# Optimization experiments

Measured on AMD Instinct MI355X. Metric: run time of the kernel, lower is better.

Reference implementation:

```python
import jax, jax.numpy as jnp
import numpy as np
import math

NH, DH, BS, LOCAL, RAND, NCLS = 12, 64, 49, 3, 3, 1
WINDOW = (8, 14, 14)
NKV = LOCAL + RAND


def make_rel_pos_index():
    ws = WINDOW
    rel_size = [2 * w - 1 for w in ws]
    coords = np.stack(np.meshgrid(*[np.arange(w) for w in ws], indexing='ij')).reshape(len(ws), -1)
    rel = (coords[:, :, None] - coords[:, None, :]).transpose(1, 2, 0).astype(np.int64)
    for i, w in enumerate(ws):
        rel[:, :, i] += w - 1
    for i, r in enumerate(rel_size[1:]):
        rel[:, :, :i + 1] *= r
    n = coords.shape[1]
    S = n + NCLS
    idx = np.zeros((S, S), dtype=np.int64)
    idx[NCLS:, NCLS:] = rel.sum(-1)
    start = int(np.prod(rel_size))
    idx[:NCLS, NCLS:] = np.arange(NCLS)[:, None] + start
    start += NCLS
    idx[NCLS:, :NCLS] = np.arange(NCLS)[None, :] + start
    start += NCLS
    idx[:NCLS, :NCLS] = np.arange(NCLS ** 2).reshape(NCLS, NCLS) + start
    return idx.astype(np.int32)


def setup_inputs() -> dict:
    key = jax.random.key(0)
    ks = jax.random.split(key, 8)
    B, S, D = 8, 1569, 768
    M = (S - NCLS) // BS  # 32 blocks
    hidden_states = jax.random.normal(ks[0], (B, S, D), dtype=jnp.float32)
    Wq = jax.random.normal(ks[1], (D, D), dtype=jnp.float32) * 0.02
    bq = jax.random.normal(ks[2], (D,), dtype=jnp.float32) * 0.02
    Wk = jax.random.normal(ks[3], (D, D), dtype=jnp.float32) * 0.02
    Wv = jax.random.normal(ks[4], (D, D), dtype=jnp.float32) * 0.02
    bv = jax.random.normal(ks[5], (D,), dtype=jnp.float32) * 0.02
    rel_table = jax.random.normal(ks[6], (10938, NH), dtype=jnp.float32) * 0.02
    rel_pos_index = jnp.asarray(make_rel_pos_index())
    rand_idx = jnp.sort(jax.random.randint(ks[7], (M, RAND), 0, M), axis=1).astype(jnp.int32)
    return {"hidden_states": hidden_states, "Wq": Wq, "bq": bq, "Wk": Wk, "Wv": Wv,
            "bv": bv, "rel_table": rel_table, "rel_pos_index": rel_pos_index, "rand_idx": rand_idx}


def reference(hidden_states, Wq, bq, Wk, Wv, bv, rel_table, rel_pos_index, rand_idx):
    B, S, D = hidden_states.shape
    scale = 1.0 / math.sqrt(DH)
    q = hidden_states @ Wq + bq
    k = hidden_states @ Wk          # key has no bias in BeitSelfAttention
    v = hidden_states @ Wv + bv
    split = lambda x: x.reshape(B, S, NH, DH).transpose(0, 2, 1, 3)  # b h s d
    q, k, v = split(q), split(k), split(v)

    # --- dense attention for cls queries over all keys ---
    cls_q = q[:, :, :NCLS]
    sim_cls = jnp.einsum('bhid,bhjd->bhij', cls_q, k) * scale
    bias_cls = rel_table[rel_pos_index[:NCLS, :]]           # [ncls, S, H]
    sim_cls = sim_cls + bias_cls.transpose(2, 0, 1)[None]
    attn_cls = jax.nn.softmax(sim_cls, axis=-1)
    out_cls = jnp.einsum('bhij,bhjd->bhid', attn_cls, v)    # [B,H,ncls,DH]

    # --- block-sparse attention for local queries ---
    loc_q = q[:, :, NCLS:]
    cls_k, loc_k = k[:, :, :NCLS], k[:, :, NCLS:]
    cls_v, loc_v = v[:, :, :NCLS], v[:, :, NCLS:]
    N = S - NCLS
    M = N // BS  # evenly divisible -> pad_q = 0
    qb = loc_q.reshape(B, NH, M, BS, DH)
    kb = loc_k.reshape(B, NH, M, BS, DH)
    vb = loc_v.reshape(B, NH, M, BS, DH)

    # local + random key-block indices per query block: [M, NKV]
    offs = jnp.arange(-(LOCAL // 2), LOCAL // 2 + 1)
    local_idx = (jnp.arange(M)[:, None] + offs[None, :]) % M
    attn_idx = jnp.concatenate([local_idx.astype(jnp.int32), rand_idx], axis=1)

    kg = kb[:, :, attn_idx]   # [B,H,M,NKV,BS,DH]
    vg = vb[:, :, attn_idx]

    sim_loc = jnp.einsum('bhmid,bhmnjd->bhminj', qb, kg).reshape(B, NH, M, BS, NKV * BS)
    sim_c = jnp.einsum('bhmid,bhjd->bhmij', qb, cls_k)       # [B,H,M,BS,ncls]
    sim = jnp.concatenate([sim_c, sim_loc], axis=-1) * scale

    # gathered relative-position bias: query tokens are ncls..S-1 in order
    key_tok = (NCLS + attn_idx[:, :, None] * BS + jnp.arange(BS)[None, None, :]).reshape(M, NKV * BS)
    to_idx = jnp.concatenate([jnp.broadcast_to(jnp.arange(NCLS)[None], (M, NCLS)), key_tok], axis=1)
    q_rows = rel_pos_index[NCLS:].reshape(M, BS, S)
    bias_idx = jnp.take_along_axis(q_rows, jnp.broadcast_to(to_idx[:, None, :], (M, BS, to_idx.shape[1])), axis=-1)
    bias = rel_table[bias_idx]                                # [M,BS,ncls+NKV*BS,H]
    sim = sim + bias.transpose(3, 0, 1, 2)[None]

    attn = jax.nn.softmax(sim, axis=-1)
    a_cls = attn[..., :NCLS]
    a_loc = attn[..., NCLS:].reshape(B, NH, M, BS, NKV, BS)
    out_loc = jnp.einsum('bhminj,bhmnjd->bhmid', a_loc, vg) \
            + jnp.einsum('bhmic,bhcd->bhmid', a_cls, cls_v)
    out_loc = out_loc.reshape(B, NH, N, DH)

    out = jnp.concatenate([out_cls, out_loc], axis=2)         # [B,H,S,DH]
    return out.transpose(0, 2, 1, 3).reshape(B, S, D)
```

## Files before the change

### kernel.cpp

```cpp
#include <hip/hip_runtime.h>


#define S_TOT   1569
#define NBATCH  8

__global__ __launch_bounds__(256) void gemm_f32(const float* __restrict__ hs,
                                                const float* __restrict__ Wq,
                                                const float* __restrict__ Wk,
                                                const float* __restrict__ Wv,
                                                const float* __restrict__ bq,
                                                const float* __restrict__ bv,
                                                float* __restrict__ Q,
                                                float* __restrict__ K,
                                                float* __restrict__ V,
                                                int b0, int nTok) {
    __shared__ float As[128][20];
    __shared__ float Bs[16][136];
    int tid = threadIdx.x;
    int t0 = blockIdx.x * 128;
    int n0 = blockIdx.y * 128;
    int which = n0 / 768;
    int ng0 = n0 - which * 768;
    const float* W = (which == 0) ? Wq : (which == 1 ? Wk : Wv);
    const float* Xb = hs + (size_t)b0 * S_TOT * 768;

    int tr = tid >> 4;
    int tc = tid & 15;

    int sat = tid >> 2;
    int sac4 = (tid & 3) * 4;
    int sbk = tid >> 4;
    int sbn = (tid & 15) * 4;

    int scg = ((tid & 3) ^ ((sat >> 3) & 3)) * 4;
    int rswz = (tr & 3);

    int ta0 = t0 + sat;       if (ta0 >= nTok) ta0 = nTok - 1;
    int ta1 = t0 + sat + 64;  if (ta1 >= nTok) ta1 = nTok - 1;

    float acc[8][8];
#pragma unroll
    for (int i = 0; i < 8; i++)
#pragma unroll
        for (int j = 0; j < 8; j++) acc[i][j] = 0.f;

    float4 pa0, pa1, pb0, pb1;
    {
        pa0 = *(const float4*)(Xb + (size_t)ta0 * 768 + 0 + sac4);
        pa1 = *(const float4*)(Xb + (size_t)ta1 * 768 + 0 + sac4);
        const float* wr_ = W + (size_t)(0 + sbk) * 768 + ng0;
        pb0 = *(const float4*)(wr_ + sbn);
        pb1 = *(const float4*)(wr_ + 64 + sbn);
    }

    for (int k0 = 0; k0 < 768; k0 += 16) {
        *(float4*)&As[sat][scg]      = pa0;
        *(float4*)&As[sat + 64][scg] = pa1;
        *(float4*)&Bs[sbk][sbn]      = pb0;
        *(float4*)&Bs[sbk][64 + sbn] = pb1;
        __syncthreads();

        if (k0 + 16 < 768) {
            int kn = k0 + 16;
            pa0 = *(const float4*)(Xb + (size_t)ta0 * 768 + kn + sac4);
            pa1 = *(const float4*)(Xb + (size_t)ta1 * 768 + kn + sac4);
            const float* wr_ = W + (size_t)(kn + sbk) * 768 + ng0;
            pb0 = *(const float4*)(wr_ + sbn);
            pb1 = *(const float4*)(wr_ + 64 + sbn);
        }

#pragma unroll
        for (int kq = 0; kq < 4; kq++) {
            float4 xa[8];
            int rc = (kq ^ rswz) * 4;
#pragma unroll
            for (int i = 0; i < 8; i++)
                xa[i] = *(const float4*)&As[tr * 8 + i][rc];
#pragma unroll
            for (int kk = 0; kk < 4; kk++) {
                int k = kq * 4 + kk;
                float4 w0 = *(const float4*)&Bs[k][tc * 4];
                float4 w1 = *(const float4*)&Bs[k][64 + tc * 4];
#pragma unroll
                for (int i = 0; i < 8; i++) {
                    float a = (kk == 0) ? xa[i].x : (kk == 1) ? xa[i].y
                            : (kk == 2) ? xa[i].z : xa[i].w;
                    acc[i][0] = fmaf(a, w0.x, acc[i][0]);
                    acc[i][1] = fmaf(a, w0.y, acc[i][1]);
                    acc[i][2] = fmaf(a, w0.z, acc[i][2]);
                    acc[i][3] = fmaf(a, w0.w, acc[i][3]);
                    acc[i][4] = fmaf(a, w1.x, acc[i][4]);
                    acc[i][5] = fmaf(a, w1.y, acc[i][5]);
                    acc[i][6] = fmaf(a, w1.z, acc[i][6]);
                    acc[i][7] = fmaf(a, w1.w, acc[i][7]);
                }
            }
        }
        __syncthreads();
    }

    float* dst = (which == 0) ? Q : (which == 1 ? K : V);
    const float* bias = (which == 0) ? bq : (which == 2 ? bv : nullptr);
#pragma unroll
    for (int hh = 0; hh < 2; hh++) {
        int nn = ng0 + hh * 64 + tc * 4;
        int h = nn >> 6, d = nn & 63;
        float4 bv4 = make_float4(0.f, 0.f, 0.f, 0.f);
        if (bias) bv4 = *(const float4*)(bias + nn);
#pragma unroll
        for (int i = 0; i < 8; i++) {
            int t = t0 + tr * 8 + i;
            if (t >= nTok) continue;
            int bl = t / S_TOT;
            int s = t - bl * S_TOT;
            float4 o;
            o.x = acc[i][hh * 4 + 0] + bv4.x;
            o.y = acc[i][hh * 4 + 1] + bv4.y;
            o.z = acc[i][hh * 4 + 2] + bv4.z;
            o.w = acc[i][hh * 4 + 3] + bv4.w;
            *(float4*)(dst + ((size_t)(bl * 12 + h) * S_TOT + s) * 64 + d) = o;
        }
    }
}

__global__ __launch_bounds__(256) void cls_attn(const float* __restrict__ Q,
                                                const float* __restrict__ K,
                                                const float* __restrict__ V,
                                                const float* __restrict__ rel,
                                                const int* __restrict__ rpi,
                                                float* __restrict__ out, int b0) {
    int bh = blockIdx.x;
    int bl = bh / 12, h = bh - bl * 12;
    __shared__ float p[S_TOT];
    __shared__ float4 qs4[16];
    __shared__ float red[256];
    __shared__ float wred[8];
    int tid = threadIdx.x, lane = tid & 63, w = tid >> 6;
    size_t base = (size_t)bh * S_TOT * 64;
    const float* Qb = Q + base;
    const float* Kb = K + base;
    const float* Vb = V + base;
    if (tid < 64) ((float*)qs4)[tid] = Qb[tid];
    __syncthreads();

    float lmx = -1e30f;
    for (int j = tid; j < S_TOT; j += 256) {
        const float4* kr = (const float4*)(Kb + j * 64);
        float a = 0.f;
#pragma unroll
        for (int d4 = 0; d4 < 16; d4++) {
            float4 kv = kr[d4];
            float4 qv = qs4[d4];
            a = fmaf(qv.x, kv.x, a); a = fmaf(qv.y, kv.y, a);
            a = fmaf(qv.z, kv.z, a); a = fmaf(qv.w, kv.w, a);
        }
        a = a * 0.125f + rel[rpi[j] * 12 + h];
        p[j] = a;
        lmx = fmaxf(lmx, a);
    }
#pragma unroll
    for (int off = 32; off > 0; off >>= 1) lmx = fmaxf(lmx, __shfl_xor(lmx, off));
    if (lane == 0) wred[w] = lmx;
    __syncthreads();
    float mx = fmaxf(fmaxf(wred[0], wred[1]), fmaxf(wred[2], wred[3]));
    float lsum = 0.f;
    for (int j = tid; j < S_TOT; j += 256) {
        float e = __expf(p[j] - mx);
        p[j] = e;
        lsum += e;
    }
#pragma unroll
    for (int off = 32; off > 0; off >>= 1) lsum += __shfl_xor(lsum, off);
    if (lane == 0) wred[4 + w] = lsum;
    __syncthreads();
    float inv = 1.0f / (wred[4] + wred[5] + wred[6] + wred[7]);
    float acc = 0.f;
    for (int j = w; j < S_TOT; j += 4) acc = fmaf(p[j], Vb[j * 64 + lane], acc);
    red[w * 64 + lane] = acc;
    __syncthreads();
    if (w == 0) {
        float o = (red[lane] + red[64 + lane] + red[128 + lane] + red[192 + lane]) * inv;
        out[(size_t)(b0 + bl) * S_TOT * 768 + h * 64 + lane] = o;
    }
}

__global__ __launch_bounds__(256, 4) void loc_attn(const float* __restrict__ Q,
                                                   const float* __restrict__ K,
                                                   const float* __restrict__ V,
                                                   const float* __restrict__ rel,
                                                   const int* __restrict__ rand_idx,
                                                   float* __restrict__ out,
                                                   int b0, int ng) {
    int d = blockIdx.x;
    int xcd = d & 7, kk_ = d >> 3;
    int slot = xcd * (ng << 2) + kk_;
    int g = slot >> 5;
    int m = slot & 31;
    int h = g % 12;
    int bl = g / 12;

    __shared__ float Qlds[49][64];
    __shared__ float Plds[4][13][64];
    __shared__ float flds[4][13][5];
    __shared__ int   cqlds[52];
    __shared__ unsigned short tok[320];
    int tid = threadIdx.x, lane = tid & 63, w = tid >> 6;

    size_t base = (size_t)((bl * 12 + h) * S_TOT) * 64;
    const float* Qb = Q + base;
    const float* Kb = K + base;
    const float* Vb = V + base;

    for (int jj = tid; jj < 320; jj += 256) {
        int t = 0;
        if (jj >= 1 && jj < 295) {
            int j1 = jj - 1;
            int n = j1 / 49;
            int q = j1 - n * 49;
            int a;
            if (n == 0)      a = (m + 31) & 31;
            else if (n == 1) a = m;
            else if (n == 2) a = (m + 1) & 31;
            else             a = rand_idx[m * 3 + (n - 3)];
            t = 1 + a * 49 + q;
        }
        tok[jj] = (unsigned short)t;
    }
    if (tid < 52) {
        int qr = 1 + m * 49 + tid;
        if (qr > S_TOT - 1) qr = S_TOT - 1;
        int pq = qr - 1;
        int zq = pq / 196;
        int rem = pq - zq * 196;
        int yq = rem / 14;
        int xq = rem - yq * 14;
        cqlds[tid] = zq * 729 + yq * 27 + xq;
    }
    for (int idx = tid; idx < 49 * 64; idx += 256) {
        int r = idx >> 6, c = idx & 63;
        ((float*)Qlds)[idx] = Qb[(size_t)(1 + m * 49 + r) * 64 + c];
    }
    __syncthreads();

    float facc[13];
#pragma unroll
    for (int r = 0; r < 13; r++) facc[r] = 0.f;

    for (int jc = 0; jc < 5; jc++) {
        int j = jc * 64 + lane;
        int tj = tok[j];
        const float* kp = Kb + (size_t)tj * 64;

        int pj = tj - 1;
        int zj = pj / 196;
        int remj = pj - zj * 196;
        int yj = remj / 14;
        int xj = remj - yj * 14;
        int cjb = 5467 - (zj * 729 + yj * 27 + xj);
        bool iscls = (tj == 0);
        bool jv = j < 295;

#pragma unroll
        for (int half = 0; half < 2; half++) {
            const int r0 = half * 7;
            const int RN = half ? 6 : 7;
            float s[7];
#pragma unroll
            for (int rr = 0; rr < 7; rr++) s[rr] = 0.f;
#pragma unroll 4
            for (int d4 = 0; d4 < 16; d4++) {
                float4 kv = *(const float4*)(kp + d4 * 4);
#pragma unroll
                for (int rr = 0; rr < RN; rr++) {
                    int qrow = w + 4 * (r0 + rr);
                    if (qrow > 48) qrow = 48;
                    float4 qv = *(const float4*)&Qlds[qrow][d4 * 4];
                    s[rr] = fmaf(qv.x, kv.x, s[rr]);
                    s[rr] = fmaf(qv.y, kv.y, s[rr]);
                    s[rr] = fmaf(qv.z, kv.z, s[rr]);
                    s[rr] = fmaf(qv.w, kv.w, s[rr]);
                }
            }
#pragma unroll
            for (int rr = 0; rr < RN; rr++) {
                int r = r0 + rr;
                int i = w + 4 * r;
                int ii = (i > 48) ? 48 : i;
                int bidx = iscls ? 10936 : (cqlds[ii] + cjb);
                float e = jv ? __expf(fmaf(s[rr], 0.125f, rel[bidx * 12 + h])) : 0.f;
                float ps = e;
#pragma unroll
                for (int off = 32; off > 0; off >>= 1) ps += __shfl_xor(ps, off);
                if (lane == 0) flds[w][r][jc] = ps;
                Plds[w][r][lane] = e;
            }
        }

#pragma unroll 4
        for (int jg = 0; jg < 16; jg++) {
            int jb = jc * 64 + jg * 4;
            int t0 = tok[jb + 0], t1 = tok[jb + 1], t2 = tok[jb + 2], t3 = tok[jb + 3];
            float v0 = Vb[(size_t)t0 * 64 + lane];
            float v1 = Vb[(size_t)t1 * 64 + lane];
            float v2 = Vb[(size_t)t2 * 64 + lane];
            float v3 = Vb[(size_t)t3 * 64 + lane];
#pragma unroll
            for (int r = 0; r < 13; r++) {
                float4 p4 = *(const float4*)&Plds[w][r][jg * 4];
                facc[r] = fmaf(p4.x, v0, facc[r]);
                facc[r] = fmaf(p4.y, v1, facc[r]);
                facc[r] = fmaf(p4.z, v2, facc[r]);
                facc[r] = fmaf(p4.w, v3, facc[r]);
            }
        }
    }

    int nrows = (w == 0) ? 13 : 12;
    for (int r = 0; r < nrows; r++) {
        float fl = ((flds[w][r][0] + flds[w][r][1]) + (flds[w][r][2] + flds[w][r][3]))
                 + flds[w][r][4];
        int i = w + 4 * r;
        int st = 1 + m * 49 + i;
        out[((size_t)(b0 + bl) * S_TOT + st) * 768 + h * 64 + lane] = facc[r] / fl;
    }
}

extern "C" void kernel_launch(void* const* d_in, const int* in_sizes, int n_in,
                              void* d_out, int out_size, void* d_ws, size_t ws_size,
                              hipStream_t stream) {
    (void)in_sizes; (void)n_in; (void)out_size;
    const float* hs  = (const float*)d_in[0];
    const float* Wq  = (const float*)d_in[1];
    const float* bq  = (const float*)d_in[2];
    const float* Wk  = (const float*)d_in[3];
    const float* Wv  = (const float*)d_in[4];
    const float* bv  = (const float*)d_in[5];
    const float* rel = (const float*)d_in[6];
    const int*   rpi = (const int*)d_in[7];
    const int*   rnd = (const int*)d_in[8];
    float* out = (float*)d_out;
    char* ws = (char*)d_ws;

    constexpr size_t PBUF = (size_t)12 * S_TOT * 64 * 4;

    int C = 1;
    if (ws_size >= 3 * PBUF) {
        size_t c = ws_size / (3 * PBUF);
        C = (c >= NBATCH) ? NBATCH : (int)c;
        if (C < 1) C = 1;
    }
    float* Q = (float*)(ws);
    float* K = (float*)(ws + (size_t)C * PBUF);
    float* V = (float*)(ws + (size_t)C * PBUF * 2);

    for (int b0 = 0; b0 < NBATCH; b0 += C) {
        int cb = (NBATCH - b0 < C) ? (NBATCH - b0) : C;
        int nTok = cb * S_TOT;
        gemm_f32<<<dim3((nTok + 127) / 128, 18), dim3(256), 0, stream>>>(
            hs, Wq, Wk, Wv, bq, bv, Q, K, V, b0, nTok);
        cls_attn<<<dim3(12 * cb), dim3(256), 0, stream>>>(Q, K, V, rel, rpi, out, b0);
        int ngrp = 12 * cb;
        loc_attn<<<dim3(32 * ngrp), dim3(256), 0, stream>>>(
            Q, K, V, rel, rnd, out, b0, ngrp);
    }
}
```

Measured before the change: 1.163 ms.

## Make GEMM persistent and fuse CLS and local attention into one launch

The QKV GEMM becomes a grid-stride persistent kernel with a 1D grid capped at 1536 blocks, each looping over 128x128 output tiles. The separate CLS-attention and local-attention kernels are merged into one launch: blocks past the local range run the CLS path, and the two paths share LDS through a union. This removes one kernel launch and lets the few long CLS blocks run alongside local blocks instead of serially. The persistent GEMM may load-balance differently and could lose occupancy, and the union sizes LDS to the larger of the two layouts.

```diff
diff --git a/kernel.cpp b/kernel.cpp
--- a/kernel.cpp
+++ b/kernel.cpp
@@ -17,11 +17,6 @@
     __shared__ float As[128][20];
     __shared__ float Bs[16][136];
     int tid = threadIdx.x;
-    int t0 = blockIdx.x * 128;
-    int n0 = blockIdx.y * 128;
-    int which = n0 / 768;
-    int ng0 = n0 - which * 768;
-    const float* W = (which == 0) ? Wq : (which == 1 ? Wk : Wv);
     const float* Xb = hs + (size_t)b0 * S_TOT * 768;
 
     int tr = tid >> 4;
@@ -35,176 +30,194 @@
     int scg = ((tid & 3) ^ ((sat >> 3) & 3)) * 4;
     int rswz = (tr & 3);
 
-    int ta0 = t0 + sat;       if (ta0 >= nTok) ta0 = nTok - 1;
-    int ta1 = t0 + sat + 64;  if (ta1 >= nTok) ta1 = nTok - 1;
-
-    float acc[8][8];
-#pragma unroll
-    for (int i = 0; i < 8; i++)
-#pragma unroll
-        for (int j = 0; j < 8; j++) acc[i][j] = 0.f;
-
-    float4 pa0, pa1, pb0, pb1;
-    {
-        pa0 = *(const float4*)(Xb + (size_t)ta0 * 768 + 0 + sac4);
-        pa1 = *(const float4*)(Xb + (size_t)ta1 * 768 + 0 + sac4);
-        const float* wr_ = W + (size_t)(0 + sbk) * 768 + ng0;
-        pb0 = *(const float4*)(wr_ + sbn);
-        pb1 = *(const float4*)(wr_ + 64 + sbn);
-    }
-
-    for (int k0 = 0; k0 < 768; k0 += 16) {
-        *(float4*)&As[sat][scg]      = pa0;
-        *(float4*)&As[sat + 64][scg] = pa1;
-        *(float4*)&Bs[sbk][sbn]      = pb0;
-        *(float4*)&Bs[sbk][64 + sbn] = pb1;
-        __syncthreads();
-
-        if (k0 + 16 < 768) {
-            int kn = k0 + 16;
-            pa0 = *(const float4*)(Xb + (size_t)ta0 * 768 + kn + sac4);
-            pa1 = *(const float4*)(Xb + (size_t)ta1 * 768 + kn + sac4);
-            const float* wr_ = W + (size_t)(kn + sbk) * 768 + ng0;
+    int ntt = (nTok + 127) >> 7;
+    int ntiles = ntt * 18;
+
+    for (int tile = blockIdx.x; tile < ntiles; tile += gridDim.x) {
+        int tx = tile / 18;
+        int ty = tile - tx * 18;
+        int t0 = tx << 7;
+        int n0 = ty << 7;
+        int which = n0 / 768;
+        int ng0 = n0 - which * 768;
+        const float* W = (which == 0) ? Wq : (which == 1 ? Wk : Wv);
+
+        int ta0 = t0 + sat;       if (ta0 >= nTok) ta0 = nTok - 1;
+        int ta1 = t0 + sat + 64;  if (ta1 >= nTok) ta1 = nTok - 1;
+
+        float acc[8][8];
+#pragma unroll
+        for (int i = 0; i < 8; i++)
+#pragma unroll
+            for (int j = 0; j < 8; j++) acc[i][j] = 0.f;
+
+        float4 pa0, pa1, pb0, pb1;
+        {
+            pa0 = *(const float4*)(Xb + (size_t)ta0 * 768 + 0 + sac4);
+            pa1 = *(const float4*)(Xb + (size_t)ta1 * 768 + 0 + sac4);
+            const float* wr_ = W + (size_t)(0 + sbk) * 768 + ng0;
             pb0 = *(const float4*)(wr_ + sbn);
             pb1 = *(const float4*)(wr_ + 64 + sbn);
         }
 
-#pragma unroll
-        for (int kq = 0; kq < 4; kq++) {
-            float4 xa[8];
-            int rc = (kq ^ rswz) * 4;
-#pragma unroll
-            for (int i = 0; i < 8; i++)
-                xa[i] = *(const float4*)&As[tr * 8 + i][rc];
-#pragma unroll
-            for (int kk = 0; kk < 4; kk++) {
-                int k = kq * 4 + kk;
-                float4 w0 = *(const float4*)&Bs[k][tc * 4];
-                float4 w1 = *(const float4*)&Bs[k][64 + tc * 4];
-#pragma unroll
-                for (int i = 0; i < 8; i++) {
-                    float a = (kk == 0) ? xa[i].x : (kk == 1) ? xa[i].y
-                            : (kk == 2) ? xa[i].z : xa[i].w;
-                    acc[i][0] = fmaf(a, w0.x, acc[i][0]);
-                    acc[i][1] = fmaf(a, w0.y, acc[i][1]);
-                    acc[i][2] = fmaf(a, w0.z, acc[i][2]);
-                    acc[i][3] = fmaf(a, w0.w, acc[i][3]);
-                    acc[i][4] = fmaf(a, w1.x, acc[i][4]);
-                    acc[i][5] = fmaf(a, w1.y, acc[i][5]);
-                    acc[i][6] = fmaf(a, w1.z, acc[i][6]);
-                    acc[i][7] = fmaf(a, w1.w, acc[i][7]);
+        for (int k0 = 0; k0 < 768; k0 += 16) {
+            *(float4*)&As[sat][scg]      = pa0;
+            *(float4*)&As[sat + 64][scg] = pa1;
+            *(float4*)&Bs[sbk][sbn]      = pb0;
+            *(float4*)&Bs[sbk][64 + sbn] = pb1;
+            __syncthreads();
+
+            if (k0 + 16 < 768) {
+                int kn = k0 + 16;
+                pa0 = *(const float4*)(Xb + (size_t)ta0 * 768 + kn + sac4);
+                pa1 = *(const float4*)(Xb + (size_t)ta1 * 768 + kn + sac4);
+                const float* wr_ = W + (size_t)(kn + sbk) * 768 + ng0;
+                pb0 = *(const float4*)(wr_ + sbn);
+                pb1 = *(const float4*)(wr_ + 64 + sbn);
+            }
+
+#pragma unroll
+            for (int kq = 0; kq < 4; kq++) {
+                float4 xa[8];
+                int rc = (kq ^ rswz) * 4;
+#pragma unroll
+                for (int i = 0; i < 8; i++)
+                    xa[i] = *(const float4*)&As[tr * 8 + i][rc];
+#pragma unroll
+                for (int kk = 0; kk < 4; kk++) {
+                    int k = kq * 4 + kk;
+                    float4 w0 = *(const float4*)&Bs[k][tc * 4];
+                    float4 w1 = *(const float4*)&Bs[k][64 + tc * 4];
+#pragma unroll
+                    for (int i = 0; i < 8; i++) {
+                        float a = (kk == 0) ? xa[i].x : (kk == 1) ? xa[i].y
+                                : (kk == 2) ? xa[i].z : xa[i].w;
+                        acc[i][0] = fmaf(a, w0.x, acc[i][0]);
+                        acc[i][1] = fmaf(a, w0.y, acc[i][1]);
+                        acc[i][2] = fmaf(a, w0.z, acc[i][2]);
+                        acc[i][3] = fmaf(a, w0.w, acc[i][3]);
+                        acc[i][4] = fmaf(a, w1.x, acc[i][4]);
+                        acc[i][5] = fmaf(a, w1.y, acc[i][5]);
+                        acc[i][6] = fmaf(a, w1.z, acc[i][6]);
+                        acc[i][7] = fmaf(a, w1.w, acc[i][7]);
+                    }
                 }
             }
-        }
+            __syncthreads();
+        }
+
+        float* dst = (which == 0) ? Q : (which == 1 ? K : V);
+        const float* bias = (which == 0) ? bq : (which == 2 ? bv : nullptr);
+#pragma unroll
+        for (int hh = 0; hh < 2; hh++) {
+            int nn = ng0 + hh * 64 + tc * 4;
+            int h = nn >> 6, d = nn & 63;
+            float4 bv4 = make_float4(0.f, 0.f, 0.f, 0.f);
+            if (bias) bv4 = *(const float4*)(bias + nn);
+#pragma unroll
+            for (int i = 0; i < 8; i++) {
+                int t = t0 + tr * 8 + i;
+                if (t >= nTok) continue;
+                int bl = t / S_TOT;
+                int s = t - bl * S_TOT;
+                float4 o;
+                o.x = acc[i][hh * 4 + 0] + bv4.x;
+                o.y = acc[i][hh * 4 + 1] + bv4.y;
+                o.z = acc[i][hh * 4 + 2] + bv4.z;
+                o.w = acc[i][hh * 4 + 3] + bv4.w;
+                *(float4*)(dst + ((size_t)(bl * 12 + h) * S_TOT + s) * 64 + d) = o;
+            }
+        }
+    }
+}
+
+struct LocS {
+    float Qlds[49][64];
+    float Plds[4][13][64];
+    float flds[4][13][5];
+    int   cqlds[52];
+    unsigned short tok[320];
+};
+struct ClsS {
+    float4 qs4[16];
+    float  p[S_TOT];
+    float  red[256];
+    float  wred[8];
+};
+union SMem { LocS loc; ClsS cls; };
+
+__global__ __launch_bounds__(256, 4) void attn_fused(const float* __restrict__ Q,
+                                                     const float* __restrict__ K,
+                                                     const float* __restrict__ V,
+                                                     const float* __restrict__ rel,
+                                                     const int* __restrict__ rpi,
+                                                     const int* __restrict__ rand_idx,
+                                                     float* __restrict__ out,
+                                                     int b0, int ng) {
+    __shared__ SMem sm;
+    int tid = threadIdx.x, lane = tid & 63, w = tid >> 6;
+    int dd = blockIdx.x;
+
+    if (dd >= 32 * ng) {
+        int bh = dd - 32 * ng;
+        int bl = bh / 12, h = bh - bl * 12;
+        size_t base = (size_t)bh * S_TOT * 64;
+        const float* Qb = Q + base;
+        const float* Kb = K + base;
+        const float* Vb = V + base;
+        if (tid < 64) ((float*)sm.cls.qs4)[tid] = Qb[tid];
         __syncthreads();
-    }
-
-    float* dst = (which == 0) ? Q : (which == 1 ? K : V);
-    const float* bias = (which == 0) ? bq : (which == 2 ? bv : nullptr);
-#pragma unroll
-    for (int hh = 0; hh < 2; hh++) {
-        int nn = ng0 + hh * 64 + tc * 4;
-        int h = nn >> 6, d = nn & 63;
-        float4 bv4 = make_float4(0.f, 0.f, 0.f, 0.f);
-        if (bias) bv4 = *(const float4*)(bias + nn);
-#pragma unroll
-        for (int i = 0; i < 8; i++) {
-            int t = t0 + tr * 8 + i;
-            if (t >= nTok) continue;
-            int bl = t / S_TOT;
-            int s = t - bl * S_TOT;
-            float4 o;
-            o.x = acc[i][hh * 4 + 0] + bv4.x;
-            o.y = acc[i][hh * 4 + 1] + bv4.y;
-            o.z = acc[i][hh * 4 + 2] + bv4.z;
-            o.w = acc[i][hh * 4 + 3] + bv4.w;
-            *(float4*)(dst + ((size_t)(bl * 12 + h) * S_TOT + s) * 64 + d) = o;
-        }
-    }
-}
-
-__global__ __launch_bounds__(256) void cls_attn(const float* __restrict__ Q,
-                                                const float* __restrict__ K,
-                                                const float* __restrict__ V,
-                                                const float* __restrict__ rel,
-                                                const int* __restrict__ rpi,
-                                                float* __restrict__ out, int b0) {
-    int bh = blockIdx.x;
-    int bl = bh / 12, h = bh - bl * 12;
-    __shared__ float p[S_TOT];
-    __shared__ float4 qs4[16];
-    __shared__ float red[256];
-    __shared__ float wred[8];
-    int tid = threadIdx.x, lane = tid & 63, w = tid >> 6;
-    size_t base = (size_t)bh * S_TOT * 64;
-    const float* Qb = Q + base;
-    const float* Kb = K + base;
-    const float* Vb = V + base;
-    if (tid < 64) ((float*)qs4)[tid] = Qb[tid];
-    __syncthreads();
-
-    float lmx = -1e30f;
-    for (int j = tid; j < S_TOT; j += 256) {
-        const float4* kr = (const float4*)(Kb + j * 64);
-        float a = 0.f;
-#pragma unroll
-        for (int d4 = 0; d4 < 16; d4++) {
-            float4 kv = kr[d4];
-            float4 qv = qs4[d4];
-            a = fmaf(qv.x, kv.x, a); a = fmaf(qv.y, kv.y, a);
-            a = fmaf(qv.z, kv.z, a); a = fmaf(qv.w, kv.w, a);
-        }
-        a = a * 0.125f + rel[rpi[j] * 12 + h];
-        p[j] = a;
-        lmx = fmaxf(lmx, a);
-    }
-#pragma unroll
-    for (int off = 32; off > 0; off >>= 1) lmx = fmaxf(lmx, __shfl_xor(lmx, off));
-    if (lane == 0) wred[w] = lmx;
-    __syncthreads();
-    float mx = fmaxf(fmaxf(wred[0], wred[1]), fmaxf(wred[2], wred[3]));
-    float lsum = 0.f;
-    for (int j = tid; j < S_TOT; j += 256) {
-        float e = __expf(p[j] - mx);
-        p[j] = e;
-        lsum += e;
-    }
-#pragma unroll
-    for (int off = 32; off > 0; off >>= 1) lsum += __shfl_xor(lsum, off);
-    if (lane == 0) wred[4 + w] = lsum;
-    __syncthreads();
-    float inv = 1.0f / (wred[4] + wred[5] + wred[6] + wred[7]);
-    float acc = 0.f;
-    for (int j = w; j < S_TOT; j += 4) acc = fmaf(p[j], Vb[j * 64 + lane], acc);
-    red[w * 64 + lane] = acc;
-    __syncthreads();
-    if (w == 0) {
-        float o = (red[lane] + red[64 + lane] + red[128 + lane] + red[192 + lane]) * inv;
-        out[(size_t)(b0 + bl) * S_TOT * 768 + h * 64 + lane] = o;
-    }
-}
-
-__global__ __launch_bounds__(256, 4) void loc_attn(const float* __restrict__ Q,
-                                                   const float* __restrict__ K,
-                                                   const float* __restrict__ V,
-                                                   const float* __restrict__ rel,
-                                                   const int* __restrict__ rand_idx,
-                                                   float* __restrict__ out,
-                                                   int b0, int ng) {
-    int d = blockIdx.x;
-    int xcd = d & 7, kk_ = d >> 3;
+
+        float lmx = -1e30f;
+        for (int j = tid; j < S_TOT; j += 256) {
+            const float4* kr = (const float4*)(Kb + j * 64);
+            float a = 0.f;
+#pragma unroll
+            for (int d4 = 0; d4 < 16; d4++) {
+                float4 kv = kr[d4];
+                float4 qv = sm.cls.qs4[d4];
+                a = fmaf(qv.x, kv.x, a); a = fmaf(qv.y, kv.y, a);
+                a = fmaf(qv.z, kv.z, a); a = fmaf(qv.w, kv.w, a);
+            }
+            a = a * 0.125f + rel[rpi[j] * 12 + h];
+            sm.cls.p[j] = a;
+            lmx = fmaxf(lmx, a);
+        }
+#pragma unroll
+        for (int off = 32; off > 0; off >>= 1) lmx = fmaxf(lmx, __shfl_xor(lmx, off));
+        if (lane == 0) sm.cls.wred[w] = lmx;
+        __syncthreads();
+        float mx = fmaxf(fmaxf(sm.cls.wred[0], sm.cls.wred[1]),
+                         fmaxf(sm.cls.wred[2], sm.cls.wred[3]));
+        float lsum = 0.f;
+        for (int j = tid; j < S_TOT; j += 256) {
+            float e = __expf(sm.cls.p[j] - mx);
+            sm.cls.p[j] = e;
+            lsum += e;
+        }
+#pragma unroll
+        for (int off = 32; off > 0; off >>= 1) lsum += __shfl_xor(lsum, off);
+        if (lane == 0) sm.cls.wred[4 + w] = lsum;
+        __syncthreads();
+        float inv = 1.0f / (sm.cls.wred[4] + sm.cls.wred[5] + sm.cls.wred[6] + sm.cls.wred[7]);
+        float acc = 0.f;
+        for (int j = w; j < S_TOT; j += 4) acc = fmaf(sm.cls.p[j], Vb[j * 64 + lane], acc);
+        sm.cls.red[w * 64 + lane] = acc;
+        __syncthreads();
+        if (w == 0) {
+            float o = (sm.cls.red[lane] + sm.cls.red[64 + lane] +
+                       sm.cls.red[128 + lane] + sm.cls.red[192 + lane]) * inv;
+            out[(size_t)(b0 + bl) * S_TOT * 768 + h * 64 + lane] = o;
+        }
+        return;
+    }
+
+    int xcd = dd & 7, kk_ = dd >> 3;
     int slot = xcd * (ng << 2) + kk_;
     int g = slot >> 5;
     int m = slot & 31;
     int h = g % 12;
     int bl = g / 12;
-
-    __shared__ float Qlds[49][64];
-    __shared__ float Plds[4][13][64];
-    __shared__ float flds[4][13][5];
-    __shared__ int   cqlds[52];
-    __shared__ unsigned short tok[320];
-    int tid = threadIdx.x, lane = tid & 63, w = tid >> 6;
 
     size_t base = (size_t)((bl * 12 + h) * S_TOT) * 64;
     const float* Qb = Q + base;
@@ -224,7 +237,7 @@
             else             a = rand_idx[m * 3 + (n - 3)];
             t = 1 + a * 49 + q;
         }
-        tok[jj] = (unsigned short)t;
+        sm.loc.tok[jj] = (unsigned short)t;
     }
     if (tid < 52) {
         int qr = 1 + m * 49 + tid;
@@ -234,11 +247,11 @@
         int rem = pq - zq * 196;
         int yq = rem / 14;
         int xq = rem - yq * 14;
-        cqlds[tid] = zq * 729 + yq * 27 + xq;
+        sm.loc.cqlds[tid] = zq * 729 + yq * 27 + xq;
     }
     for (int idx = tid; idx < 49 * 64; idx += 256) {
         int r = idx >> 6, c = idx & 63;
-        ((float*)Qlds)[idx] = Qb[(size_t)(1 + m * 49 + r) * 64 + c];
+        ((float*)sm.loc.Qlds)[idx] = Qb[(size_t)(1 + m * 49 + r) * 64 + c];
     }
     __syncthreads();
 
@@ -248,7 +261,7 @@
 
     for (int jc = 0; jc < 5; jc++) {
         int j = jc * 64 + lane;
-        int tj = tok[j];
+        int tj = sm.loc.tok[j];
         const float* kp = Kb + (size_t)tj * 64;
 
         int pj = tj - 1;
@@ -274,7 +287,7 @@
                 for (int rr = 0; rr < RN; rr++) {
                     int qrow = w + 4 * (r0 + rr);
                     if (qrow > 48) qrow = 48;
-                    float4 qv = *(const float4*)&Qlds[qrow][d4 * 4];
+                    float4 qv = *(const float4*)&sm.loc.Qlds[qrow][d4 * 4];
                     s[rr] = fmaf(qv.x, kv.x, s[rr]);
                     s[rr] = fmaf(qv.y, kv.y, s[rr]);
                     s[rr] = fmaf(qv.z, kv.z, s[rr]);
@@ -286,27 +299,28 @@
                 int r = r0 + rr;
                 int i = w + 4 * r;
                 int ii = (i > 48) ? 48 : i;
-                int bidx = iscls ? 10936 : (cqlds[ii] + cjb);
+                int bidx = iscls ? 10936 : (sm.loc.cqlds[ii] + cjb);
                 float e = jv ? __expf(fmaf(s[rr], 0.125f, rel[bidx * 12 + h])) : 0.f;
                 float ps = e;
 #pragma unroll
                 for (int off = 32; off > 0; off >>= 1) ps += __shfl_xor(ps, off);
-                if (lane == 0) flds[w][r][jc] = ps;
-                Plds[w][r][lane] = e;
+                if (lane == 0) sm.loc.flds[w][r][jc] = ps;
+                sm.loc.Plds[w][r][lane] = e;
             }
         }
 
 #pragma unroll 4
         for (int jg = 0; jg < 16; jg++) {
             int jb = jc * 64 + jg * 4;
-            int t0 = tok[jb + 0], t1 = tok[jb + 1], t2 = tok[jb + 2], t3 = tok[jb + 3];
+            int t0 = sm.loc.tok[jb + 0], t1 = sm.loc.tok[jb + 1];
+            int t2 = sm.loc.tok[jb + 2], t3 = sm.loc.tok[jb + 3];
             float v0 = Vb[(size_t)t0 * 64 + lane];
             float v1 = Vb[(size_t)t1 * 64 + lane];
             float v2 = Vb[(size_t)t2 * 64 + lane];
             float v3 = Vb[(size_t)t3 * 64 + lane];
 #pragma unroll
             for (int r = 0; r < 13; r++) {
-                float4 p4 = *(const float4*)&Plds[w][r][jg * 4];
+                float4 p4 = *(const float4*)&sm.loc.Plds[w][r][jg * 4];
                 facc[r] = fmaf(p4.x, v0, facc[r]);
                 facc[r] = fmaf(p4.y, v1, facc[r]);
                 facc[r] = fmaf(p4.z, v2, facc[r]);
@@ -317,8 +331,9 @@
 
     int nrows = (w == 0) ? 13 : 12;
     for (int r = 0; r < nrows; r++) {
-        float fl = ((flds[w][r][0] + flds[w][r][1]) + (flds[w][r][2] + flds[w][r][3]))
-                 + flds[w][r][4];
+        float fl = ((sm.loc.flds[w][r][0] + sm.loc.flds[w][r][1]) +
+                    (sm.loc.flds[w][r][2] + sm.loc.flds[w][r][3]))
+                 + sm.loc.flds[w][r][4];
         int i = w + 4 * r;
         int st = 1 + m * 49 + i;
         out[((size_t)(b0 + bl) * S_TOT + st) * 768 + h * 64 + lane] = facc[r] / fl;
@@ -356,11 +371,12 @@
     for (int b0 = 0; b0 < NBATCH; b0 += C) {
         int cb = (NBATCH - b0 < C) ? (NBATCH - b0) : C;
         int nTok = cb * S_TOT;
-        gemm_f32<<<dim3((nTok + 127) / 128, 18), dim3(256), 0, stream>>>(
+        int ntiles = ((nTok + 127) / 128) * 18;
+        int gsz = (ntiles < 1536) ? ntiles : 1536;
+        gemm_f32<<<dim3(gsz), dim3(256), 0, stream>>>(
             hs, Wq, Wk, Wv, bq, bv, Q, K, V, b0, nTok);
-        cls_attn<<<dim3(12 * cb), dim3(256), 0, stream>>>(Q, K, V, rel, rpi, out, b0);
         int ngrp = 12 * cb;
-        loc_attn<<<dim3(32 * ngrp), dim3(256), 0, stream>>>(
-            Q, K, V, rel, rnd, out, b0, ngrp);
+        attn_fused<<<dim3(33 * ngrp), dim3(256), 0, stream>>>(
+            Q, K, V, rel, rpi, rnd, out, b0, ngrp);
     }
 }
```

Result: faster. 1.088 ms (-6.4%).
